# Performance work log

Hardware: AMD Instinct MI355X
Metric: run time of the kernel (lower is better)

Reference implementation:

```python
import jax, jax.numpy as jnp
import numpy as np

B, N, F_IN, F_OUT = 8, 2048, 128, 128
NEG_BIG = -9e15
LEAKY_SLOPE = 0.01


def setup_inputs() -> dict:
    key = jax.random.key(0)
    k1, k2, k3, k4, k5 = jax.random.split(key, 5)
    features = jax.random.normal(k1, (B, N, F_IN), dtype=jnp.float32)
    adj_matrix = jax.random.randint(k2, (B, N, N), 0, 2, dtype=jnp.int32)
    mask = jnp.ones((B, N), dtype=jnp.float32)
    # linear: W [in,out], b [out]; attention: a [2*out] (no bias)
    W = jax.random.normal(k3, (F_IN, F_OUT), dtype=jnp.float32) / np.sqrt(F_IN)
    b = jnp.zeros((F_OUT,), dtype=jnp.float32)
    a = jax.random.normal(k4, (2 * F_OUT,), dtype=jnp.float32) / np.sqrt(2 * F_OUT)
    return {"features": features, "adj_matrix": adj_matrix, "mask": mask,
            "W": W, "b": b, "a": a}


def reference(features, adj_matrix, mask, W, b, a):
    h = jnp.einsum("bni,io->bno", features, W) + b  # [B,N,F_OUT]
    # attention(concat([h_i, h_j])) == h_i @ a_src + h_j @ a_dst
    a_src, a_dst = a[:F_OUT], a[F_OUT:]
    e = (h @ a_src)[:, :, None] + (h @ a_dst)[:, None, :]  # [B,N,N]
    e = jnp.where(e >= 0, e, LEAKY_SLOPE * e)  # leaky_relu
    scores = jnp.where(adj_matrix > 0, e, jnp.float32(NEG_BIG))
    attention = jax.nn.softmax(scores, axis=-1)
    aggregated = jnp.einsum("bnm,bmo->bno", attention, h)  # [B,N,F_OUT]
    aggregated = aggregated * mask[:, :, None]
    return aggregated
```

## Files before the change

### kernel.cpp

```cpp
#include <hip/hip_runtime.h>

#define BB 8
#define NN 2048
#define FF 128
#define RB 16
#define MT 128

typedef short bh8 __attribute__((ext_vector_type(8)));
typedef float fl4 __attribute__((ext_vector_type(4)));
typedef unsigned short u16;

__device__ __forceinline__ u16 f2bf(float x) {
    unsigned u = __float_as_uint(x);
    return (u16)((u + 0x7FFFu + ((u >> 16) & 1u)) >> 16);
}

__global__ __launch_bounds__(256) void k_h(
    const float* __restrict__ feat, const float* __restrict__ W,
    const float* __restrict__ bias, const float* __restrict__ a,
    u16* __restrict__ htg, float* __restrict__ esrc, float* __restrict__ edst)
{
    __shared__ float fsh[8][FF];
    __shared__ float red[2][2][8];
    const int t = threadIdx.x;
    const long row0 = (long)blockIdx.x * 8;

    ((float4*)&fsh[0][0])[t] = ((const float4*)(feat + row0 * FF))[t];
    __syncthreads();

    const int o = t & 127;
    const int half = t >> 7;
    float acc[4] = {0.f, 0.f, 0.f, 0.f};
    #pragma unroll 4
    for (int k = 0; k < FF; ++k) {
        const float w = W[k * FF + o];
        #pragma unroll
        for (int r = 0; r < 4; ++r)
            acc[r] = fmaf(fsh[half * 4 + r][k], w, acc[r]);
    }
    const float bo = bias[o];
    const float as = a[o];
    const float ad = a[FF + o];
    float ps[4], pd[4];
    #pragma unroll
    for (int r = 0; r < 4; ++r) {
        acc[r] += bo;
        ps[r] = acc[r] * as;
        pd[r] = acc[r] * ad;
    }
    {
        const int bI = (int)(row0 >> 11);
        const int nloc = (int)(row0 & 2047) + half * 4;
        ushort4 hv;
        hv.x = f2bf(acc[0]); hv.y = f2bf(acc[1]);
        hv.z = f2bf(acc[2]); hv.w = f2bf(acc[3]);
        *(ushort4*)&htg[((long)bI * FF + o) * NN + nloc] = hv;
    }
    #pragma unroll
    for (int r = 0; r < 4; ++r) {
        #pragma unroll
        for (int off = 32; off > 0; off >>= 1) {
            ps[r] += __shfl_down(ps[r], off, 64);
            pd[r] += __shfl_down(pd[r], off, 64);
        }
    }
    const int wv = (t >> 6) & 1;
    if ((t & 63) == 0) {
        #pragma unroll
        for (int r = 0; r < 4; ++r) {
            red[half][wv][r]     = ps[r];
            red[half][wv][4 + r] = pd[r];
        }
    }
    __syncthreads();
    if (t < 16) {
        const int hh = t >> 3, idx = t & 7;
        const float v = red[hh][0][idx] + red[hh][1][idx];
        const long row = row0 + hh * 4 + (idx & 3);
        if (idx < 4) esrc[row] = v;
        else         edst[row] = v;
    }
}

__global__ __launch_bounds__(256, 4) void k_attn(
    const int* __restrict__ adj, const float* __restrict__ mask,
    const u16* __restrict__ htg, const float* __restrict__ esrc,
    const float* __restrict__ edst, float* __restrict__ out)
{
    __shared__ float accbuf[4][RB][FF];
    __shared__ float psum_sh[4][RB];

    const int t = threadIdx.x;
    const int b = blockIdx.x & 7;
    const int n0 = (blockIdx.x >> 3) * RB;
    const int w = t >> 6, lane = t & 63;
    const int lr = lane & 15, g = lane >> 4;

    float gmx = -3.4e38f;
    {
        const float4* edp = (const float4*)(edst + b * NN);
        #pragma unroll
        for (int i = 0; i < 8; ++i) {
            const float4 v = edp[lane + 64 * i];
            gmx = fmaxf(gmx, fmaxf(fmaxf(v.x, v.y), fmaxf(v.z, v.w)));
        }
        #pragma unroll
        for (int off = 32; off > 0; off >>= 1)
            gmx = fmaxf(gmx, __shfl_xor(gmx, off, 64));
    }

    const float es = esrc[b * NN + n0 + lr];
    const float tM = es + gmx;
    const float M = (tM >= 0.f) ? tM : 0.01f * tM;

    const long adjrow = (long)b * NN * NN + (long)(n0 + lr) * NN;
    const u16* hB = htg + (long)b * FF * NN;
    const float* edb = edst + b * NN;

    fl4 acc[8];
    #pragma unroll
    for (int ct = 0; ct < 8; ++ct) acc[ct] = (fl4){0.f, 0.f, 0.f, 0.f};
    float psum = 0.f;

    #pragma unroll 1
    for (int it = 0; it < 4; ++it) {
        const int m0 = (w + 4 * it) * MT;
        const int base = m0 + g * 8;

        int4 aj[8];
        #pragma unroll
        for (int kc = 0; kc < 4; ++kc) {
            aj[2 * kc]     = *(const int4*)(adj + adjrow + base + kc * 32);
            aj[2 * kc + 1] = *(const int4*)(adj + adjrow + base + kc * 32 + 4);
        }

        bh8 af[4];
        #pragma unroll
        for (int kc = 0; kc < 4; ++kc) {
            const float4 e0 = *(const float4*)(edb + base + kc * 32);
            const float4 e1 = *(const float4*)(edb + base + kc * 32 + 4);
            const float ee[8] = {e0.x, e0.y, e0.z, e0.w, e1.x, e1.y, e1.z, e1.w};
            const int   aa[8] = {aj[2*kc].x, aj[2*kc].y, aj[2*kc].z, aj[2*kc].w,
                                 aj[2*kc+1].x, aj[2*kc+1].y, aj[2*kc+1].z, aj[2*kc+1].w};
            u16 pb[8];
            #pragma unroll
            for (int j = 0; j < 8; ++j) {
                float x = es + ee[j];
                x = (x >= 0.f) ? x : 0.01f * x;
                const float p = (aa[j] > 0) ? __expf(x - M) : 0.f;
                const u16 ub = f2bf(p);
                pb[j] = ub;
                psum += __uint_as_float((unsigned)ub << 16);
            }
            af[kc] = (bh8){(short)pb[0], (short)pb[1], (short)pb[2], (short)pb[3],
                           (short)pb[4], (short)pb[5], (short)pb[6], (short)pb[7]};
        }

        #pragma unroll
        for (int kc = 0; kc < 4; ++kc) {
            #pragma unroll
            for (int ct = 0; ct < 8; ++ct) {
                const bh8 bf = *(const bh8*)(hB + (long)(ct * 16 + lr) * NN + base + kc * 32);
                acc[ct] = __builtin_amdgcn_mfma_f32_16x16x32_bf16(af[kc], bf, acc[ct], 0, 0, 0);
            }
        }
    }

    psum += __shfl_xor(psum, 16, 64);
    psum += __shfl_xor(psum, 32, 64);
    if (lane < 16) psum_sh[w][lane] = psum;

    #pragma unroll
    for (int ct = 0; ct < 8; ++ct)
        #pragma unroll
        for (int reg = 0; reg < 4; ++reg)
            accbuf[w][g * 4 + reg][ct * 16 + lr] = acc[ct][reg];
    __syncthreads();

    #pragma unroll
    for (int rep = 0; rep < 2; ++rep) {
        const int idx = t + 256 * rep;
        const int r = idx >> 5;
        const int c4 = (idx & 31) * 4;
        const float4 s0 = *(const float4*)&accbuf[0][r][c4];
        const float4 s1 = *(const float4*)&accbuf[1][r][c4];
        const float4 s2 = *(const float4*)&accbuf[2][r][c4];
        const float4 s3 = *(const float4*)&accbuf[3][r][c4];
        const float ps = psum_sh[0][r] + psum_sh[1][r] + psum_sh[2][r] + psum_sh[3][r];
        const float sc = mask[b * NN + n0 + r] / ps;
        float4 o;
        o.x = (s0.x + s1.x + s2.x + s3.x) * sc;
        o.y = (s0.y + s1.y + s2.y + s3.y) * sc;
        o.z = (s0.z + s1.z + s2.z + s3.z) * sc;
        o.w = (s0.w + s1.w + s2.w + s3.w) * sc;
        *(float4*)&out[((long)b * NN + n0 + r) * FF + c4] = o;
    }
}

extern "C" void kernel_launch(void* const* d_in, const int* in_sizes, int n_in,
                              void* d_out, int out_size, void* d_ws, size_t ws_size,
                              hipStream_t stream)
{
    const float* feat = (const float*)d_in[0];
    const int*   adj  = (const int*)d_in[1];
    const float* mask = (const float*)d_in[2];
    const float* W    = (const float*)d_in[3];
    const float* bias = (const float*)d_in[4];
    const float* a    = (const float*)d_in[5];
    float* out = (float*)d_out;

    u16*   htg  = (u16*)d_ws;
    float* esrc = (float*)(htg + (size_t)BB * FF * NN);
    float* edst = esrc + BB * NN;

    k_h   <<<BB * NN / 8, 256, 0, stream>>>(feat, W, bias, a, htg, esrc, edst);
    k_attn<<<BB * (NN / RB), 256, 0, stream>>>(adj, mask, htg, esrc, edst, out);
}
```

Baseline: 103.3 us.

## Pack adjacency into bitmask, double row block per workgroup, prefetch B fragments

Adds a pre-pass kernel that ballots the int32 adjacency into 64-bit bitmasks. The attention kernel then reads the compact mask instead of the full int32 matrix. RB grows to 32, so each wave reuses its h fragments for two 16-row tiles, and the h fragments and next mask words are software-prefetched. The adjacency still has to be read once in full by the pack kernel, plus one extra launch. Register pressure rises (occupancy hint drops to 2) and accbuf is padded against bank conflicts.

```diff
diff --git a/kernel.cpp b/kernel.cpp
--- a/kernel.cpp
+++ b/kernel.cpp
@@ -3,12 +3,13 @@
 #define BB 8
 #define NN 2048
 #define FF 128
-#define RB 16
+#define RB 32
 #define MT 128
 
 typedef short bh8 __attribute__((ext_vector_type(8)));
 typedef float fl4 __attribute__((ext_vector_type(4)));
 typedef unsigned short u16;
+typedef unsigned long long u64;
 
 __device__ __forceinline__ u16 f2bf(float x) {
     unsigned u = __float_as_uint(x);
@@ -82,12 +83,28 @@
     }
 }
 
-__global__ __launch_bounds__(256, 4) void k_attn(
-    const int* __restrict__ adj, const float* __restrict__ mask,
+__global__ __launch_bounds__(256) void k_pack(
+    const int* __restrict__ adj, u64* __restrict__ bm)
+{
+    const int t = threadIdx.x;
+    const int w = t >> 6, lane = t & 63;
+    const long row0 = (long)blockIdx.x * 8;
+    #pragma unroll 8
+    for (int i = 0; i < 64; ++i) {
+        const int row = 2 * w + (i >> 5);
+        const int chunk = i & 31;
+        const int av = adj[(row0 + row) * NN + chunk * 64 + lane];
+        const u64 m64 = __ballot(av > 0);
+        if (lane == 0) bm[(row0 + row) * 32 + chunk] = m64;
+    }
+}
+
+__global__ __launch_bounds__(256, 2) void k_attn(
+    const u64* __restrict__ bm, const float* __restrict__ mask,
     const u16* __restrict__ htg, const float* __restrict__ esrc,
     const float* __restrict__ edst, float* __restrict__ out)
 {
-    __shared__ float accbuf[4][RB][FF];
+    __shared__ float accbuf[4][RB][FF + 4];
     __shared__ float psum_sh[4][RB];
 
     const int t = threadIdx.x;
@@ -109,76 +126,116 @@
             gmx = fmaxf(gmx, __shfl_xor(gmx, off, 64));
     }
 
-    const float es = esrc[b * NN + n0 + lr];
-    const float tM = es + gmx;
-    const float M = (tM >= 0.f) ? tM : 0.01f * tM;
-
-    const long adjrow = (long)b * NN * NN + (long)(n0 + lr) * NN;
+    const float es0 = esrc[b * NN + n0 + lr];
+    const float es1 = esrc[b * NN + n0 + 16 + lr];
+    const float tA = es0 + gmx; const float M0 = (tA >= 0.f) ? tA : 0.01f * tA;
+    const float tB = es1 + gmx; const float M1 = (tB >= 0.f) ? tB : 0.01f * tB;
+
+    const uint4* bmb = (const uint4*)(bm + ((long)b * NN + n0) * 32);
+    const float* edb = edst + b * NN;
     const u16* hB = htg + (long)b * FF * NN;
-    const float* edb = edst + b * NN;
-
-    fl4 acc[8];
-    #pragma unroll
-    for (int ct = 0; ct < 8; ++ct) acc[ct] = (fl4){0.f, 0.f, 0.f, 0.f};
-    float psum = 0.f;
+
+    fl4 acc0[8], acc1[8];
+    #pragma unroll
+    for (int ct = 0; ct < 8; ++ct) {
+        acc0[ct] = (fl4){0.f, 0.f, 0.f, 0.f};
+        acc1[ct] = (fl4){0.f, 0.f, 0.f, 0.f};
+    }
+    float psum0 = 0.f, psum1 = 0.f;
+
+    uint4 bmA0 = bmb[lr * 16 + w];
+    uint4 bmA1 = bmb[(16 + lr) * 16 + w];
 
     #pragma unroll 1
     for (int it = 0; it < 4; ++it) {
         const int m0 = (w + 4 * it) * MT;
         const int base = m0 + g * 8;
 
-        int4 aj[8];
+        float4 ed[8];
         #pragma unroll
         for (int kc = 0; kc < 4; ++kc) {
-            aj[2 * kc]     = *(const int4*)(adj + adjrow + base + kc * 32);
-            aj[2 * kc + 1] = *(const int4*)(adj + adjrow + base + kc * 32 + 4);
-        }
-
-        bh8 af[4];
+            ed[2 * kc]     = *(const float4*)(edb + base + kc * 32);
+            ed[2 * kc + 1] = *(const float4*)(edb + base + kc * 32 + 4);
+        }
+        bh8 bfA[8];
+        #pragma unroll
+        for (int ct = 0; ct < 8; ++ct)
+            bfA[ct] = *(const bh8*)(hB + (long)(ct * 16 + lr) * NN + base);
+        const int itn = (it + 1) & 3;
+        uint4 bmB0 = bmb[lr * 16 + w + 4 * itn];
+        uint4 bmB1 = bmb[(16 + lr) * 16 + w + 4 * itn];
+
+        bh8 af0[4], af1[4];
         #pragma unroll
         for (int kc = 0; kc < 4; ++kc) {
-            const float4 e0 = *(const float4*)(edb + base + kc * 32);
-            const float4 e1 = *(const float4*)(edb + base + kc * 32 + 4);
+            const unsigned w0 = (kc == 0) ? bmA0.x : (kc == 1) ? bmA0.y
+                              : (kc == 2) ? bmA0.z : bmA0.w;
+            const unsigned w1 = (kc == 0) ? bmA1.x : (kc == 1) ? bmA1.y
+                              : (kc == 2) ? bmA1.z : bmA1.w;
+            const unsigned by0 = (w0 >> (8 * g)) & 0xFFu;
+            const unsigned by1 = (w1 >> (8 * g)) & 0xFFu;
+            const float4 e0 = ed[2 * kc], e1 = ed[2 * kc + 1];
             const float ee[8] = {e0.x, e0.y, e0.z, e0.w, e1.x, e1.y, e1.z, e1.w};
-            const int   aa[8] = {aj[2*kc].x, aj[2*kc].y, aj[2*kc].z, aj[2*kc].w,
-                                 aj[2*kc+1].x, aj[2*kc+1].y, aj[2*kc+1].z, aj[2*kc+1].w};
-            u16 pb[8];
+            u16 p0[8], p1[8];
             #pragma unroll
             for (int j = 0; j < 8; ++j) {
-                float x = es + ee[j];
-                x = (x >= 0.f) ? x : 0.01f * x;
-                const float p = (aa[j] > 0) ? __expf(x - M) : 0.f;
-                const u16 ub = f2bf(p);
-                pb[j] = ub;
-                psum += __uint_as_float((unsigned)ub << 16);
-            }
-            af[kc] = (bh8){(short)pb[0], (short)pb[1], (short)pb[2], (short)pb[3],
-                           (short)pb[4], (short)pb[5], (short)pb[6], (short)pb[7]};
+                float x0 = es0 + ee[j]; x0 = (x0 >= 0.f) ? x0 : 0.01f * x0;
+                float x1 = es1 + ee[j]; x1 = (x1 >= 0.f) ? x1 : 0.01f * x1;
+                const float v0 = ((by0 >> j) & 1u) ? __expf(x0 - M0) : 0.f;
+                const float v1 = ((by1 >> j) & 1u) ? __expf(x1 - M1) : 0.f;
+                const u16 u0 = f2bf(v0), u1 = f2bf(v1);
+                p0[j] = u0; p1[j] = u1;
+                psum0 += __uint_as_float((unsigned)u0 << 16);
+                psum1 += __uint_as_float((unsigned)u1 << 16);
+            }
+            af0[kc] = (bh8){(short)p0[0], (short)p0[1], (short)p0[2], (short)p0[3],
+                            (short)p0[4], (short)p0[5], (short)p0[6], (short)p0[7]};
+            af1[kc] = (bh8){(short)p1[0], (short)p1[1], (short)p1[2], (short)p1[3],
+                            (short)p1[4], (short)p1[5], (short)p1[6], (short)p1[7]};
         }
 
         #pragma unroll
         for (int kc = 0; kc < 4; ++kc) {
+            bh8 bfB[8];
+            if (kc < 3) {
+                #pragma unroll
+                for (int ct = 0; ct < 8; ++ct)
+                    bfB[ct] = *(const bh8*)(hB + (long)(ct * 16 + lr) * NN
+                                            + base + (kc + 1) * 32);
+            }
             #pragma unroll
             for (int ct = 0; ct < 8; ++ct) {
-                const bh8 bf = *(const bh8*)(hB + (long)(ct * 16 + lr) * NN + base + kc * 32);
-                acc[ct] = __builtin_amdgcn_mfma_f32_16x16x32_bf16(af[kc], bf, acc[ct], 0, 0, 0);
-            }
-        }
-    }
-
-    psum += __shfl_xor(psum, 16, 64);
-    psum += __shfl_xor(psum, 32, 64);
-    if (lane < 16) psum_sh[w][lane] = psum;
+                acc0[ct] = __builtin_amdgcn_mfma_f32_16x16x32_bf16(af0[kc], bfA[ct], acc0[ct], 0, 0, 0);
+                acc1[ct] = __builtin_amdgcn_mfma_f32_16x16x32_bf16(af1[kc], bfA[ct], acc1[ct], 0, 0, 0);
+            }
+            if (kc < 3) {
+                #pragma unroll
+                for (int ct = 0; ct < 8; ++ct) bfA[ct] = bfB[ct];
+            }
+        }
+        bmA0 = bmB0; bmA1 = bmB1;
+    }
+
+    psum0 += __shfl_xor(psum0, 16, 64);
+    psum0 += __shfl_xor(psum0, 32, 64);
+    psum1 += __shfl_xor(psum1, 16, 64);
+    psum1 += __shfl_xor(psum1, 32, 64);
+    if (lane < 16) {
+        psum_sh[w][lr] = psum0;
+        psum_sh[w][16 + lr] = psum1;
+    }
 
     #pragma unroll
     for (int ct = 0; ct < 8; ++ct)
         #pragma unroll
-        for (int reg = 0; reg < 4; ++reg)
-            accbuf[w][g * 4 + reg][ct * 16 + lr] = acc[ct][reg];
+        for (int reg = 0; reg < 4; ++reg) {
+            accbuf[w][g * 4 + reg][ct * 16 + lr]      = acc0[ct][reg];
+            accbuf[w][16 + g * 4 + reg][ct * 16 + lr] = acc1[ct][reg];
+        }
     __syncthreads();
 
     #pragma unroll
-    for (int rep = 0; rep < 2; ++rep) {
+    for (int rep = 0; rep < 4; ++rep) {
         const int idx = t + 256 * rep;
         const int r = idx >> 5;
         const int c4 = (idx & 31) * 4;
@@ -212,7 +269,9 @@
     u16*   htg  = (u16*)d_ws;
     float* esrc = (float*)(htg + (size_t)BB * FF * NN);
     float* edst = esrc + BB * NN;
-
+    u64*   bmp  = (u64*)(edst + BB * NN);
+
+    k_pack<<<BB * NN / 8, 256, 0, stream>>>(adj, bmp);
     k_h   <<<BB * NN / 8, 256, 0, stream>>>(feat, W, bias, a, htg, esrc, edst);
-    k_attn<<<BB * (NN / RB), 256, 0, stream>>>(adj, mask, htg, esrc, edst, out);
-}
+    k_attn<<<BB * (NN / RB), 256, 0, stream>>>(bmp, mask, htg, esrc, edst, out);
+}
```

Result: faster. 86.15 us (-16.6%).

## Pack adjacency to bitmask, factor exp, stage H in LDS with double buffering

Applied to the files above, without the earlier changes.

Adds a pre-pass that packs the int32 adjacency into 64-bit bitmasks, which k_attn then reads instead of the raw int matrix. The exponential is factored into per-row and per-column terms, exp(es-M)*exp(ed) and exp(0.01es-M)*exp(0.01ed), with a max between them, so the inner loop has no exp. The attention kernel now takes 64 rows per block, with each wave owning 16 rows over the full column range. Each 128-column window of H is staged in swizzled, double-buffered LDS, which removes the cross-wave reduction. The packing kernel still reads the whole 134MB adjacency, so total traffic is not reduced. The factored products could overflow or underflow where direct exp did not.

```diff
diff --git a/kernel.cpp b/kernel.cpp
--- a/kernel.cpp
+++ b/kernel.cpp
@@ -3,22 +3,39 @@
 #define BB 8
 #define NN 2048
 #define FF 128
-#define RB 16
 #define MT 128
 
 typedef short bh8 __attribute__((ext_vector_type(8)));
 typedef float fl4 __attribute__((ext_vector_type(4)));
 typedef unsigned short u16;
+typedef unsigned long long u64;
 
 __device__ __forceinline__ u16 f2bf(float x) {
     unsigned u = __float_as_uint(x);
     return (u16)((u + 0x7FFFu + ((u >> 16) & 1u)) >> 16);
 }
 
+__global__ __launch_bounds__(256) void k_pack(
+    const int* __restrict__ adj, u64* __restrict__ bm)
+{
+    const long gt = (long)blockIdx.x * 256 + threadIdx.x;
+    const int4* src = (const int4*)adj + gt * 16;
+    u64 m = 0;
+    #pragma unroll
+    for (int i = 0; i < 16; ++i) {
+        const int4 v = src[i];
+        const unsigned nib = (v.x > 0 ? 1u : 0u) | (v.y > 0 ? 2u : 0u)
+                           | (v.z > 0 ? 4u : 0u) | (v.w > 0 ? 8u : 0u);
+        m |= (u64)nib << (4 * i);
+    }
+    bm[gt] = m;
+}
+
 __global__ __launch_bounds__(256) void k_h(
     const float* __restrict__ feat, const float* __restrict__ W,
     const float* __restrict__ bias, const float* __restrict__ a,
-    u16* __restrict__ htg, float* __restrict__ esrc, float* __restrict__ edst)
+    u16* __restrict__ htg, float* __restrict__ esrc, float* __restrict__ edst,
+    float* __restrict__ eed, float* __restrict__ eed2)
 {
     __shared__ float fsh[8][FF];
     __shared__ float red[2][2][8];
@@ -77,22 +94,27 @@
         const int hh = t >> 3, idx = t & 7;
         const float v = red[hh][0][idx] + red[hh][1][idx];
         const long row = row0 + hh * 4 + (idx & 3);
-        if (idx < 4) esrc[row] = v;
-        else         edst[row] = v;
-    }
-}
-
-__global__ __launch_bounds__(256, 4) void k_attn(
-    const int* __restrict__ adj, const float* __restrict__ mask,
+        if (idx < 4) {
+            esrc[row] = v;
+        } else {
+            edst[row] = v;
+            eed[row]  = __expf(v);
+            eed2[row] = __expf(0.01f * v);
+        }
+    }
+}
+
+__global__ __launch_bounds__(256, 1) void k_attn(
+    const u64* __restrict__ bm, const float* __restrict__ mask,
     const u16* __restrict__ htg, const float* __restrict__ esrc,
-    const float* __restrict__ edst, float* __restrict__ out)
-{
-    __shared__ float accbuf[4][RB][FF];
-    __shared__ float psum_sh[4][RB];
+    const float* __restrict__ edst, const float* __restrict__ eed,
+    const float* __restrict__ eed2, float* __restrict__ out)
+{
+    __shared__ u16 Hs[2][128][128];
 
     const int t = threadIdx.x;
     const int b = blockIdx.x & 7;
-    const int n0 = (blockIdx.x >> 3) * RB;
+    const int n0 = (blockIdx.x >> 3) * 64;
     const int w = t >> 6, lane = t & 63;
     const int lr = lane & 15, g = lane >> 4;
 
@@ -109,91 +131,107 @@
             gmx = fmaxf(gmx, __shfl_xor(gmx, off, 64));
     }
 
-    const float es = esrc[b * NN + n0 + lr];
-    const float tM = es + gmx;
-    const float M = (tM >= 0.f) ? tM : 0.01f * tM;
-
-    const long adjrow = (long)b * NN * NN + (long)(n0 + lr) * NN;
-    const u16* hB = htg + (long)b * FF * NN;
-    const float* edb = edst + b * NN;
+    const int myrow = n0 + w * 16 + lr;
+    const float es = esrc[b * NN + myrow];
+    const float mt = es + gmx;
+    const float M = fmaxf(mt, 0.01f * mt);
+    const float A  = __expf(es - M);
+    const float Bv = __expf(0.01f * es - M);
+
+    const uint4*  bmb  = (const uint4*)(bm + (long)b * NN * 32);
+    const float4* eebw = (const float4*)(eed + b * NN);
+    const float4* ee2w = (const float4*)(eed2 + b * NN);
+    const u16*    htgB = htg + (long)b * FF * NN;
+
+    const int srow   = t >> 4;
+    const int schunk = (t & 15) ^ (srow & 7);
+    const u16* sbase = htgB + srow * NN + schunk * 8;
 
     fl4 acc[8];
     #pragma unroll
     for (int ct = 0; ct < 8; ++ct) acc[ct] = (fl4){0.f, 0.f, 0.f, 0.f};
     float psum = 0.f;
 
+    {
+        float4 hr[8];
+        #pragma unroll
+        for (int i = 0; i < 8; ++i)
+            hr[i] = *(const float4*)(sbase + (long)i * 16 * NN);
+        u16* hd = &Hs[0][0][0];
+        #pragma unroll
+        for (int i = 0; i < 8; ++i)
+            *(float4*)(hd + i * 2048 + t * 8) = hr[i];
+    }
+    uint4 bqA = bmb[myrow * 16];
+    __syncthreads();
+
+    int cur = 0;
     #pragma unroll 1
-    for (int it = 0; it < 4; ++it) {
-        const int m0 = (w + 4 * it) * MT;
-        const int base = m0 + g * 8;
-
-        int4 aj[8];
+    for (int win = 0; win < 16; ++win) {
+        const int wn = (win + 1) & 15;
+
+        float4 hr[8];
+        #pragma unroll
+        for (int i = 0; i < 8; ++i)
+            hr[i] = *(const float4*)(sbase + (long)i * 16 * NN + wn * MT);
+
+        const uint4 bqB = bmb[myrow * 16 + wn];
+
+        bh8 af[4];
         #pragma unroll
         for (int kc = 0; kc < 4; ++kc) {
-            aj[2 * kc]     = *(const int4*)(adj + adjrow + base + kc * 32);
-            aj[2 * kc + 1] = *(const int4*)(adj + adjrow + base + kc * 32 + 4);
-        }
-
-        bh8 af[4];
-        #pragma unroll
-        for (int kc = 0; kc < 4; ++kc) {
-            const float4 e0 = *(const float4*)(edb + base + kc * 32);
-            const float4 e1 = *(const float4*)(edb + base + kc * 32 + 4);
-            const float ee[8] = {e0.x, e0.y, e0.z, e0.w, e1.x, e1.y, e1.z, e1.w};
-            const int   aa[8] = {aj[2*kc].x, aj[2*kc].y, aj[2*kc].z, aj[2*kc].w,
-                                 aj[2*kc+1].x, aj[2*kc+1].y, aj[2*kc+1].z, aj[2*kc+1].w};
-            u16 pb[8];
+            const unsigned q = (kc == 0) ? bqA.x : (kc == 1) ? bqA.y
+                             : (kc == 2) ? bqA.z : bqA.w;
+            const unsigned by = (q >> (8 * g)) & 0xFFu;
+            const float4 Ea = eebw[win * 32 + kc * 8 + g * 2];
+            const float4 Eb = eebw[win * 32 + kc * 8 + g * 2 + 1];
+            const float4 Fa = ee2w[win * 32 + kc * 8 + g * 2];
+            const float4 Fb = ee2w[win * 32 + kc * 8 + g * 2 + 1];
+            const float pe[8] = {Ea.x, Ea.y, Ea.z, Ea.w, Eb.x, Eb.y, Eb.z, Eb.w};
+            const float pf[8] = {Fa.x, Fa.y, Fa.z, Fa.w, Fb.x, Fb.y, Fb.z, Fb.w};
             #pragma unroll
             for (int j = 0; j < 8; ++j) {
-                float x = es + ee[j];
-                x = (x >= 0.f) ? x : 0.01f * x;
-                const float p = (aa[j] > 0) ? __expf(x - M) : 0.f;
-                const u16 ub = f2bf(p);
-                pb[j] = ub;
+                const float v = ((by >> j) & 1u)
+                              ? fmaxf(A * pe[j], Bv * pf[j]) : 0.f;
+                const u16 ub = f2bf(v);
+                af[kc][j] = (short)ub;
                 psum += __uint_as_float((unsigned)ub << 16);
             }
-            af[kc] = (bh8){(short)pb[0], (short)pb[1], (short)pb[2], (short)pb[3],
-                           (short)pb[4], (short)pb[5], (short)pb[6], (short)pb[7]};
         }
 
         #pragma unroll
         for (int kc = 0; kc < 4; ++kc) {
+            const int ch = ((kc << 2) + g) ^ (lr & 7);
             #pragma unroll
             for (int ct = 0; ct < 8; ++ct) {
-                const bh8 bf = *(const bh8*)(hB + (long)(ct * 16 + lr) * NN + base + kc * 32);
+                const bh8 bf = *(const bh8*)&Hs[cur][ct * 16 + lr][ch * 8];
                 acc[ct] = __builtin_amdgcn_mfma_f32_16x16x32_bf16(af[kc], bf, acc[ct], 0, 0, 0);
             }
         }
+
+        {
+            u16* hd = &Hs[cur ^ 1][0][0];
+            #pragma unroll
+            for (int i = 0; i < 8; ++i)
+                *(float4*)(hd + i * 2048 + t * 8) = hr[i];
+        }
+        __syncthreads();
+        bqA = bqB;
+        cur ^= 1;
     }
 
     psum += __shfl_xor(psum, 16, 64);
     psum += __shfl_xor(psum, 32, 64);
-    if (lane < 16) psum_sh[w][lane] = psum;
-
-    #pragma unroll
-    for (int ct = 0; ct < 8; ++ct)
-        #pragma unroll
-        for (int reg = 0; reg < 4; ++reg)
-            accbuf[w][g * 4 + reg][ct * 16 + lr] = acc[ct][reg];
-    __syncthreads();
-
-    #pragma unroll
-    for (int rep = 0; rep < 2; ++rep) {
-        const int idx = t + 256 * rep;
-        const int r = idx >> 5;
-        const int c4 = (idx & 31) * 4;
-        const float4 s0 = *(const float4*)&accbuf[0][r][c4];
-        const float4 s1 = *(const float4*)&accbuf[1][r][c4];
-        const float4 s2 = *(const float4*)&accbuf[2][r][c4];
-        const float4 s3 = *(const float4*)&accbuf[3][r][c4];
-        const float ps = psum_sh[0][r] + psum_sh[1][r] + psum_sh[2][r] + psum_sh[3][r];
-        const float sc = mask[b * NN + n0 + r] / ps;
-        float4 o;
-        o.x = (s0.x + s1.x + s2.x + s3.x) * sc;
-        o.y = (s0.y + s1.y + s2.y + s3.y) * sc;
-        o.z = (s0.z + s1.z + s2.z + s3.z) * sc;
-        o.w = (s0.w + s1.w + s2.w + s3.w) * sc;
-        *(float4*)&out[((long)b * NN + n0 + r) * FF + c4] = o;
+
+    const long obase = ((long)b * NN + n0 + w * 16) * FF;
+    #pragma unroll
+    for (int reg = 0; reg < 4; ++reg) {
+        const int r = g * 4 + reg;
+        const float pr = __shfl(psum, r, 64);
+        const float sc = mask[b * NN + n0 + w * 16 + r] / pr;
+        #pragma unroll
+        for (int ct = 0; ct < 8; ++ct)
+            out[obase + (long)r * FF + ct * 16 + lr] = acc[ct][reg] * sc;
     }
 }
 
@@ -212,7 +250,11 @@
     u16*   htg  = (u16*)d_ws;
     float* esrc = (float*)(htg + (size_t)BB * FF * NN);
     float* edst = esrc + BB * NN;
-
-    k_h   <<<BB * NN / 8, 256, 0, stream>>>(feat, W, bias, a, htg, esrc, edst);
-    k_attn<<<BB * (NN / RB), 256, 0, stream>>>(adj, mask, htg, esrc, edst, out);
-}
+    float* eed  = edst + BB * NN;
+    float* eed2 = eed + BB * NN;
+    u64*   bmp  = (u64*)(eed2 + BB * NN);
+
+    k_pack<<<BB * NN * NN / 64 / 256, 256, 0, stream>>>(adj, bmp);
+    k_h   <<<BB * NN / 8, 256, 0, stream>>>(feat, W, bias, a, htg, esrc, edst, eed, eed2);
+    k_attn<<<BB * (NN / 64), 256, 0, stream>>>(bmp, mask, htg, esrc, edst, eed, eed2, out);
+}
```

Result: slower. 107.6 us (+4.1%).

## Pack adjacency into bitmask, double-buffer B loads, compute row sums via MFMA

Applied to the files above, without the earlier changes.

Adds a separate pass that packs the int32 adjacency into 64-bit ballot bitmasks, which the attention kernel then reads instead of the full int matrix. The attention loop is restructured into a fully unrolled, software-pipelined sequence that prefetches the next h tile and edst values into double buffers. The softmax denominator is now accumulated with an extra MFMA against a ones vector instead of scalar adds and shuffles. Padding is added to the shared accumulation buffer, and occupancy hints are reduced. The attention kernel reads far less, but the pack pass still reads the full adjacency, so total traffic is not lowered much and an extra launch is added.

```diff
diff --git a/kernel.cpp b/kernel.cpp
--- a/kernel.cpp
+++ b/kernel.cpp
@@ -1,18 +1,41 @@
 #include <hip/hip_runtime.h>
+#include <hip/hip_bf16.h>
 
 #define BB 8
 #define NN 2048
 #define FF 128
-#define RB 16
-#define MT 128
 
 typedef short bh8 __attribute__((ext_vector_type(8)));
 typedef float fl4 __attribute__((ext_vector_type(4)));
 typedef unsigned short u16;
+typedef unsigned long long u64;
+typedef union { bh8 v; unsigned u[4]; } bh8u;
 
 __device__ __forceinline__ u16 f2bf(float x) {
     unsigned u = __float_as_uint(x);
     return (u16)((u + 0x7FFFu + ((u >> 16) & 1u)) >> 16);
+}
+
+__device__ __forceinline__ void loadB(bh8 (&buf)[8], const u16* hB, int lr, int kbase) {
+    #pragma unroll
+    for (int ct = 0; ct < 8; ++ct)
+        buf[ct] = *(const bh8*)(hB + (ct * 16 + lr) * NN + kbase);
+}
+
+__global__ __launch_bounds__(256) void k_pack(
+    const int* __restrict__ adj, u64* __restrict__ bm)
+{
+    const int t = threadIdx.x;
+    const int w = t >> 6, lane = t & 63;
+    const long row0 = (long)blockIdx.x * 8;
+    #pragma unroll 8
+    for (int i = 0; i < 64; ++i) {
+        const int row = 2 * w + (i >> 5);
+        const int chunk = i & 31;
+        const int av = adj[(row0 + row) * NN + chunk * 64 + lane];
+        const u64 m64 = __ballot(av > 0);
+        if (lane == 0) bm[(row0 + row) * 32 + chunk] = m64;
+    }
 }
 
 __global__ __launch_bounds__(256) void k_h(
@@ -82,26 +105,26 @@
     }
 }
 
-__global__ __launch_bounds__(256, 4) void k_attn(
-    const int* __restrict__ adj, const float* __restrict__ mask,
+__global__ __launch_bounds__(256, 3) void k_attn(
+    const u64* __restrict__ bm, const float* __restrict__ mask,
     const u16* __restrict__ htg, const float* __restrict__ esrc,
     const float* __restrict__ edst, float* __restrict__ out)
 {
-    __shared__ float accbuf[4][RB][FF];
-    __shared__ float psum_sh[4][RB];
+    __shared__ float accbuf[4][16][FF + 4];
+    __shared__ float psum_sh[4][16];
 
     const int t = threadIdx.x;
     const int b = blockIdx.x & 7;
-    const int n0 = (blockIdx.x >> 3) * RB;
+    const int n0 = (blockIdx.x >> 3) * 16;
     const int w = t >> 6, lane = t & 63;
     const int lr = lane & 15, g = lane >> 4;
 
     float gmx = -3.4e38f;
     {
-        const float4* edp = (const float4*)(edst + b * NN);
+        const float4* edp4 = (const float4*)(edst + b * NN);
         #pragma unroll
         for (int i = 0; i < 8; ++i) {
-            const float4 v = edp[lane + 64 * i];
+            const float4 v = edp4[lane + 64 * i];
             gmx = fmaxf(gmx, fmaxf(fmaxf(v.x, v.y), fmaxf(v.z, v.w)));
         }
         #pragma unroll
@@ -110,66 +133,80 @@
     }
 
     const float es = esrc[b * NN + n0 + lr];
-    const float tM = es + gmx;
-    const float M = (tM >= 0.f) ? tM : 0.01f * tM;
-
-    const long adjrow = (long)b * NN * NN + (long)(n0 + lr) * NN;
-    const u16* hB = htg + (long)b * FF * NN;
+    const float mt0 = es + gmx;
+    const float M = fmaxf(mt0, 0.01f * mt0);
+
+    const u16*   hB  = htg + (long)b * FF * NN;
     const float* edb = edst + b * NN;
+    const uint4* bmrow = (const uint4*)(bm + ((long)b * NN + n0 + lr) * 32);
+
+    const int mq = w * 512;
 
     fl4 acc[8];
     #pragma unroll
     for (int ct = 0; ct < 8; ++ct) acc[ct] = (fl4){0.f, 0.f, 0.f, 0.f};
-    float psum = 0.f;
-
-    #pragma unroll 1
+    fl4 accs = (fl4){0.f, 0.f, 0.f, 0.f};
+    const bh8 ones = {(short)0x3F80, (short)0x3F80, (short)0x3F80, (short)0x3F80,
+                      (short)0x3F80, (short)0x3F80, (short)0x3F80, (short)0x3F80};
+
+    bh8    bfb[2][8];
+    float4 edq[2][2];
+    uint4  bq[2];
+
+    loadB(bfb[0], hB, lr, mq + g * 8);
+    edq[0][0] = *(const float4*)(edb + mq + g * 8);
+    edq[0][1] = *(const float4*)(edb + mq + g * 8 + 4);
+    bq[0] = bmrow[w * 4];
+
+    #pragma unroll
     for (int it = 0; it < 4; ++it) {
-        const int m0 = (w + 4 * it) * MT;
-        const int base = m0 + g * 8;
-
-        int4 aj[8];
         #pragma unroll
         for (int kc = 0; kc < 4; ++kc) {
-            aj[2 * kc]     = *(const int4*)(adj + adjrow + base + kc * 32);
-            aj[2 * kc + 1] = *(const int4*)(adj + adjrow + base + kc * 32 + 4);
-        }
-
-        bh8 af[4];
-        #pragma unroll
-        for (int kc = 0; kc < 4; ++kc) {
-            const float4 e0 = *(const float4*)(edb + base + kc * 32);
-            const float4 e1 = *(const float4*)(edb + base + kc * 32 + 4);
-            const float ee[8] = {e0.x, e0.y, e0.z, e0.w, e1.x, e1.y, e1.z, e1.w};
-            const int   aa[8] = {aj[2*kc].x, aj[2*kc].y, aj[2*kc].z, aj[2*kc].w,
-                                 aj[2*kc+1].x, aj[2*kc+1].y, aj[2*kc+1].z, aj[2*kc+1].w};
-            u16 pb[8];
+            const int s = it * 4 + kc;
+            const int p = s & 1, pn = p ^ 1;
+
+            if (s < 15) {
+                const int sn = s + 1;
+                const int basen = mq + (sn >> 2) * 128 + (sn & 3) * 32 + g * 8;
+                loadB(bfb[pn], hB, lr, basen);
+                edq[pn][0] = *(const float4*)(edb + basen);
+                edq[pn][1] = *(const float4*)(edb + basen + 4);
+                if ((sn & 3) == 0) bq[(sn >> 2) & 1] = bmrow[w * 4 + (sn >> 2)];
+            }
+
+            const uint4 bqc = bq[it & 1];
+            const unsigned q = (kc == 0) ? bqc.x : (kc == 1) ? bqc.y
+                             : (kc == 2) ? bqc.z : bqc.w;
+            const unsigned by = (q >> (8 * g)) & 0xFFu;
+            const float4 e0 = edq[p][0], e1 = edq[p][1];
+            const float pe[8] = {e0.x, e0.y, e0.z, e0.w, e1.x, e1.y, e1.z, e1.w};
+            bh8u pa;
             #pragma unroll
-            for (int j = 0; j < 8; ++j) {
-                float x = es + ee[j];
-                x = (x >= 0.f) ? x : 0.01f * x;
-                const float p = (aa[j] > 0) ? __expf(x - M) : 0.f;
-                const u16 ub = f2bf(p);
-                pb[j] = ub;
-                psum += __uint_as_float((unsigned)ub << 16);
+            for (int jj = 0; jj < 4; ++jj) {
+                const int j0 = 2 * jj, j1 = j0 + 1;
+                const float x0 = es + pe[j0];
+                const float x1 = es + pe[j1];
+                const float l0 = fmaxf(x0, 0.01f * x0);
+                const float l1 = fmaxf(x1, 0.01f * x1);
+                const float v0 = ((by >> j0) & 1u) ? __expf(l0 - M) : 0.f;
+                const float v1 = ((by >> j1) & 1u) ? __expf(l1 - M) : 0.f;
+                float2 cf; cf.x = v0; cf.y = v1;
+                __hip_bfloat162 r2 = __float22bfloat162_rn(cf);
+                pa.u[jj] = *reinterpret_cast<unsigned*>(&r2);
             }
-            af[kc] = (bh8){(short)pb[0], (short)pb[1], (short)pb[2], (short)pb[3],
-                           (short)pb[4], (short)pb[5], (short)pb[6], (short)pb[7]};
-        }
-
-        #pragma unroll
-        for (int kc = 0; kc < 4; ++kc) {
+
             #pragma unroll
-            for (int ct = 0; ct < 8; ++ct) {
-                const bh8 bf = *(const bh8*)(hB + (long)(ct * 16 + lr) * NN + base + kc * 32);
-                acc[ct] = __builtin_amdgcn_mfma_f32_16x16x32_bf16(af[kc], bf, acc[ct], 0, 0, 0);
-            }
-        }
-    }
-
-    psum += __shfl_xor(psum, 16, 64);
-    psum += __shfl_xor(psum, 32, 64);
-    if (lane < 16) psum_sh[w][lane] = psum;
-
+            for (int ct = 0; ct < 8; ++ct)
+                acc[ct] = __builtin_amdgcn_mfma_f32_16x16x32_bf16(pa.v, bfb[p][ct], acc[ct], 0, 0, 0);
+            accs = __builtin_amdgcn_mfma_f32_16x16x32_bf16(pa.v, ones, accs, 0, 0, 0);
+        }
+    }
+
+    if (lr == 0) {
+        #pragma unroll
+        for (int reg = 0; reg < 4; ++reg)
+            psum_sh[w][g * 4 + reg] = accs[reg];
+    }
     #pragma unroll
     for (int ct = 0; ct < 8; ++ct)
         #pragma unroll
@@ -212,7 +249,9 @@
     u16*   htg  = (u16*)d_ws;
     float* esrc = (float*)(htg + (size_t)BB * FF * NN);
     float* edst = esrc + BB * NN;
-
+    u64*   bmp  = (u64*)(edst + BB * NN);
+
+    k_pack<<<BB * NN / 8, 256, 0, stream>>>(adj, bmp);
     k_h   <<<BB * NN / 8, 256, 0, stream>>>(feat, W, bias, a, htg, esrc, edst);
-    k_attn<<<BB * (NN / RB), 256, 0, stream>>>(adj, mask, htg, esrc, edst, out);
-}
+    k_attn<<<BB * (NN / 16), 256, 0, stream>>>(bmp, mask, htg, esrc, edst, out);
+}
```

New measurement: 114.1 us. 1.1x slower.
